# Kernel tuning notes

Measured on AMD Instinct MI355X. Metric: run time of the kernel, lower is better.

## Reference

```python
import jax, jax.numpy as jnp
import numpy as np

N_NODES = 100000
N_EDGES = 1600000
N_GRAPHS = 512
NODE_DIM = 92
EDGE_DIM = 41
H = 64            # hidden_node_dim
NUM_CONV = 3
PRED_H = 128
BN_EPS = 1e-5


def setup_inputs() -> dict:
    key = jax.random.key(0)
    ks = jax.random.split(key, 16)
    inp = {
        "node_feats": jax.random.normal(ks[0], (N_NODES, NODE_DIM), jnp.float32),
        "edge_index": jax.random.randint(ks[1], (2, N_EDGES), 0, N_NODES, jnp.int32),
        "edge_feats": jax.random.normal(ks[2], (N_EDGES, EDGE_DIM), jnp.float32),
        "graph_id": jax.random.randint(ks[3], (N_NODES,), 0, N_GRAPHS, jnp.int32),
        # parameters (scaled like default torch init)
        "emb_W": jax.random.normal(ks[4], (NODE_DIM, H), jnp.float32) / np.sqrt(NODE_DIM),
        "emb_b": jnp.zeros((H,), jnp.float32),
        "conv_W": jax.random.normal(ks[5], (NUM_CONV, 2 * H + EDGE_DIM, 2 * H), jnp.float32) / np.sqrt(2 * H + EDGE_DIM),
        "conv_b": jnp.zeros((NUM_CONV, 2 * H), jnp.float32),
        "bn_gamma": jnp.ones((NUM_CONV, 2 * H), jnp.float32),
        "bn_beta": jnp.zeros((NUM_CONV, 2 * H), jnp.float32),
        "fc_W": jax.random.normal(ks[6], (H, PRED_H), jnp.float32) / np.sqrt(H),
        "fc_b": jnp.zeros((PRED_H,), jnp.float32),
        "out_W": jax.random.normal(ks[7], (PRED_H, 1), jnp.float32) / np.sqrt(PRED_H),
        "out_b": jnp.zeros((1,), jnp.float32),
    }
    return inp


def reference(node_feats, edge_index, edge_feats, graph_id,
              emb_W, emb_b, conv_W, conv_b, bn_gamma, bn_beta,
              fc_W, fc_b, out_W, out_b):
    src = edge_index[0]
    dst = edge_index[1]
    n_nodes = node_feats.shape[0]

    # 1. atom embedding
    h = node_feats @ emb_W + emb_b                         # [N, H]

    # 2. conv layers: gather -> linear -> batchnorm -> gated message -> scatter-add
    for l in range(NUM_CONV):
        z = jnp.concatenate([h[src], h[dst], edge_feats], axis=1)   # [E, 2H+edge_dim]
        z = z @ conv_W[l] + conv_b[l]                                # [E, 2H]
        mean = jnp.mean(z, axis=0)
        var = jnp.var(z, axis=0)                                     # biased, as torch BN training
        z = (z - mean) * jax.lax.rsqrt(var + BN_EPS) * bn_gamma[l] + bn_beta[l]
        msg = jax.nn.sigmoid(z[:, :H]) * jax.nn.softplus(z[:, H:])   # [E, H]
        h = h + jax.ops.segment_sum(msg, src, num_segments=n_nodes)

    # 3. per-crystal mean pooling
    sums = jax.ops.segment_sum(h, graph_id, num_segments=N_GRAPHS)   # [G, H]
    counts = jax.ops.segment_sum(jnp.ones((n_nodes,), h.dtype), graph_id, num_segments=N_GRAPHS)
    pooled = sums / jnp.maximum(counts, 1.0)[:, None]

    # 4. head
    out = jax.nn.softplus(pooled @ fc_W + fc_b)
    return out @ out_W + out_b                                       # [G, 1]
```

## Files before the change

kernel.cpp:

```cpp
#include <hip/hip_runtime.h>
#include <hip/hip_fp16.h>

#define NDIM 92
#define HDIM 64
#define EDIM 41
#define ZC   128
#define CIN  169
#define NB   2048

__global__ __launch_bounds__(256) void k_embed(
    const float* __restrict__ nf, const float* __restrict__ W,
    const float* __restrict__ b, float* __restrict__ h, int N)
{
    __shared__ float Wl[NDIM * HDIM];
    __shared__ float nfl[4][NDIM];
    int t = threadIdx.x;
    for (int i = t; i < NDIM * HDIM; i += 256) Wl[i] = W[i];
    int n0 = blockIdx.x * 4;
    for (int i = t; i < 4 * NDIM; i += 256) {
        int slot = i / NDIM, k = i - slot * NDIM;
        int n = n0 + slot;
        nfl[slot][k] = (n < N) ? nf[n * NDIM + k] : 0.f;
    }
    __syncthreads();
    int j = t & 63, slot = t >> 6;
    int n = n0 + slot;
    if (n >= N) return;
    float acc = b[j];
    #pragma unroll
    for (int k = 0; k < NDIM; k++) acc += nfl[slot][k] * Wl[k * HDIM + j];
    h[n * HDIM + j] = acc;
}

__global__ __launch_bounds__(256) void k_pq(
    const float* __restrict__ h, const float* __restrict__ Wl,
    float* __restrict__ PQ, int N)
{
    __shared__ float Wcat[64 * 256];
    __shared__ float hl[32 * 64];
    int t = threadIdx.x;
    for (int i = t; i < 64 * 256; i += 256) {
        int k = i >> 8, c = i & 255;
        Wcat[i] = (c < 128) ? Wl[k * 128 + c] : Wl[(64 + k) * 128 + (c - 128)];
    }
    int jg = t & 63, w = t >> 6;
    int ntiles = (N + 31) >> 5;
    for (int tile = blockIdx.x; tile < ntiles; tile += gridDim.x) {
        int nbase = tile << 5;
        __syncthreads();
        for (int i = t; i < 32 * 64; i += 256) {
            int nn = nbase + (i >> 6);
            hl[i] = (nn < N) ? h[nn * 64 + (i & 63)] : 0.f;
        }
        __syncthreads();
        float acc[8][4];
        #pragma unroll
        for (int n = 0; n < 8; n++)
            acc[n][0] = acc[n][1] = acc[n][2] = acc[n][3] = 0.f;
        for (int k = 0; k < 64; k++) {
            float4 w4 = *(const float4*)&Wcat[k * 256 + jg * 4];
            #pragma unroll
            for (int n = 0; n < 8; n++) {
                float hv = hl[(w * 8 + n) * 64 + k];
                acc[n][0] += hv * w4.x; acc[n][1] += hv * w4.y;
                acc[n][2] += hv * w4.z; acc[n][3] += hv * w4.w;
            }
        }
        #pragma unroll
        for (int n = 0; n < 8; n++) {
            int nn = nbase + w * 8 + n;
            if (nn < N)
                *(float4*)&PQ[nn * 256 + jg * 4] =
                    make_float4(acc[n][0], acc[n][1], acc[n][2], acc[n][3]);
        }
    }
}

__global__ __launch_bounds__(256) void k_passA(
    const float* __restrict__ PQ, const float* __restrict__ ef,
    const int* __restrict__ src, const int* __restrict__ dst,
    const float* __restrict__ Wl, const float* __restrict__ bias,
    __half* __restrict__ zh, float* __restrict__ partials, int E)
{
    int t = threadIdx.x;
    int lane = t & 63;
    int waveid = __builtin_amdgcn_readfirstlane(t >> 6);
    int pair = waveid >> 1;
    int jcol = ((waveid & 1) << 6) | lane;

    float wreg[EDIM];
    #pragma unroll
    for (int k = 0; k < EDIM; k++) wreg[k] = Wl[(128 + k) * 128 + jcol];
    float bj = bias[jcol];

    float psum = 0.f, psq = 0.f;
    int estep = gridDim.x * 2;
    for (int e = blockIdx.x * 2 + pair; e < E; e += estep) {
        int s = src[e], d = dst[e];
        const float* efe = ef + (size_t)e * EDIM;
        float acc0 = PQ[(size_t)s * 256 + jcol];
        float acc1 = PQ[(size_t)d * 256 + 128 + jcol] + bj;
        #pragma unroll
        for (int k = 0; k < 40; k += 2) {
            acc0 += efe[k]     * wreg[k];
            acc1 += efe[k + 1] * wreg[k + 1];
        }
        acc0 += efe[40] * wreg[40];
        float z = acc0 + acc1;
        zh[(size_t)e * 128 + jcol] = __float2half(z);
        psum += z; psq += z * z;
    }
    __shared__ float red[512];
    red[t] = psum; red[256 + t] = psq;
    __syncthreads();
    if (t < 128) {
        partials[blockIdx.x * 256 + t]       = red[t] + red[t + 128];
        partials[blockIdx.x * 256 + 128 + t] = red[256 + t] + red[256 + t + 128];
    }
}

__global__ __launch_bounds__(256) void k_red1(
    const float* __restrict__ partials, float* __restrict__ p2, int nb)
{
    int t = threadIdx.x, r = blockIdx.x;
    float s = 0.f;
    int b0 = r * 32, b1 = b0 + 32; if (b1 > nb) b1 = nb;
    for (int b = b0; b < b1; b++) s += partials[b * 256 + t];
    p2[r * 256 + t] = s;
}

__global__ __launch_bounds__(256) void k_bnstats(
    const float* __restrict__ p2, const float* __restrict__ gamma,
    const float* __restrict__ beta, float* __restrict__ bnA,
    float* __restrict__ bnC, int R, float invE)
{
    int t = threadIdx.x;
    float s = 0.f;
    for (int r = 0; r < R; r++) s += p2[r * 256 + t];
    __shared__ float red[256];
    red[t] = s;
    __syncthreads();
    if (t < 128) {
        float mean = red[t] * invE;
        float var  = red[128 + t] * invE - mean * mean;
        float a = gamma[t] * rsqrtf(var + 1e-5f);
        bnA[t] = a;
        bnC[t] = beta[t] - mean * a;
    }
}

__global__ __launch_bounds__(256) void k_passB(
    const __half* __restrict__ zh, const int* __restrict__ src,
    const float* __restrict__ bnA, const float* __restrict__ bnC,
    float* __restrict__ h, int E)
{
    int t = threadIdx.x;
    int j = t & 63, slot = t >> 6;
    float a0 = bnA[j],      c0 = bnC[j];
    float a1 = bnA[64 + j], c1 = bnC[64 + j];
    for (int e = blockIdx.x * 4 + slot; e < E; e += gridDim.x * 4) {
        float za = __half2float(zh[e * 128 + j])      * a0 + c0;
        float zb = __half2float(zh[e * 128 + 64 + j]) * a1 + c1;
        float sig = 1.f / (1.f + __expf(-za));
        float sp  = fmaxf(zb, 0.f) + log1pf(__expf(-fabsf(zb)));
        atomicAdd(&h[src[e] * 64 + j], sig * sp);
    }
}

__global__ __launch_bounds__(256) void k_pool(
    const float* __restrict__ h, const int* __restrict__ gid,
    float* __restrict__ pool, float* __restrict__ cnt, int N)
{
    int t = threadIdx.x;
    int j = t & 63, slot = t >> 6;
    int n = blockIdx.x * 4 + slot;
    if (n >= N) return;
    int g = gid[n];
    atomicAdd(&pool[g * 64 + j], h[n * 64 + j]);
    if (j == 0) atomicAdd(&cnt[g], 1.f);
}

__global__ __launch_bounds__(128) void k_head(
    const float* __restrict__ pool, const float* __restrict__ cnt,
    const float* __restrict__ fcW, const float* __restrict__ fcb,
    const float* __restrict__ outW, const float* __restrict__ outb,
    float* __restrict__ out, int G)
{
    int g = blockIdx.x, t = threadIdx.x;
    __shared__ float pl[64];
    if (t < 64) pl[t] = pool[g * 64 + t] / fmaxf(cnt[g], 1.f);
    __syncthreads();
    float acc = fcb[t];
    #pragma unroll
    for (int k = 0; k < 64; k++) acc += pl[k] * fcW[k * 128 + t];
    float sp = fmaxf(acc, 0.f) + log1pf(__expf(-fabsf(acc)));
    float v = sp * outW[t];
    __shared__ float red[128];
    red[t] = v;
    __syncthreads();
    for (int s = 64; s > 0; s >>= 1) {
        if (t < s) red[t] += red[t + s];
        __syncthreads();
    }
    if (t == 0) out[g] = red[0] + outb[0];
}

extern "C" void kernel_launch(void* const* d_in, const int* in_sizes, int n_in,
                              void* d_out, int out_size, void* d_ws, size_t ws_size,
                              hipStream_t stream)
{
    const float* nf    = (const float*)d_in[0];
    const int*   ei    = (const int*)d_in[1];
    const float* ef    = (const float*)d_in[2];
    const int*   gid   = (const int*)d_in[3];
    const float* embW  = (const float*)d_in[4];
    const float* embB  = (const float*)d_in[5];
    const float* convW = (const float*)d_in[6];
    const float* convB = (const float*)d_in[7];
    const float* gam   = (const float*)d_in[8];
    const float* bet   = (const float*)d_in[9];
    const float* fcW   = (const float*)d_in[10];
    const float* fcb   = (const float*)d_in[11];
    const float* outW  = (const float*)d_in[12];
    const float* outb  = (const float*)d_in[13];
    float* out = (float*)d_out;

    int N = in_sizes[0] / NDIM;
    int E = in_sizes[1] / 2;
    int G = out_size;
    const int* src = ei;
    const int* dst = ei + E;

    char* ws = (char*)d_ws;
    size_t off = 0;
    auto alloc = [&](size_t bytes) {
        void* p = ws + off;
        off = (off + bytes + 255) & ~(size_t)255;
        return p;
    };
    float*  h        = (float*)alloc((size_t)N * 64 * 4);
    float*  PQ       = (float*)alloc((size_t)N * 256 * 4);
    __half* zh       = (__half*)alloc((size_t)E * 128 * 2);
    float*  partials = (float*)alloc((size_t)NB * 256 * 4);
    float*  p2       = (float*)alloc((size_t)64 * 256 * 4);
    float*  bnA      = (float*)alloc(128 * 4);
    float*  bnC      = (float*)alloc(128 * 4);
    float*  pool     = (float*)alloc((size_t)G * 65 * 4);
    float*  cnt      = pool + (size_t)G * 64;

    k_embed<<<(N + 3) / 4, 256, 0, stream>>>(nf, embW, embB, h, N);

    for (int l = 0; l < 3; l++) {
        const float* Wl = convW + (size_t)l * CIN * ZC;
        k_pq<<<1024, 256, 0, stream>>>(h, Wl, PQ, N);
        k_passA<<<NB, 256, 0, stream>>>(PQ, ef, src, dst, Wl, convB + l * ZC,
                                        zh, partials, E);
        k_red1<<<64, 256, 0, stream>>>(partials, p2, NB);
        k_bnstats<<<1, 256, 0, stream>>>(p2, gam + l * ZC, bet + l * ZC,
                                         bnA, bnC, 64, 1.f / (float)E);
        k_passB<<<4096, 256, 0, stream>>>(zh, src, bnA, bnC, h, E);
    }

    hipMemsetAsync(pool, 0, (size_t)G * 65 * 4, stream);
    k_pool<<<(N + 3) / 4, 256, 0, stream>>>(h, gid, pool, cnt, N);
    k_head<<<G, 128, 0, stream>>>(pool, cnt, fcW, fcb, outW, outb, out, G);
}
```

Measured before the change: 4.321 ms.

## Compute edge-feature projection in passA with bf16 MFMA tiles

```diff
diff --git a/kernel.cpp b/kernel.cpp
--- a/kernel.cpp
+++ b/kernel.cpp
@@ -7,6 +7,15 @@
 #define ZC   128
 #define CIN  169
 #define NB   2048
+
+typedef __attribute__((ext_vector_type(8))) short short8;
+typedef __attribute__((ext_vector_type(4))) float f32x4;
+
+static __device__ inline unsigned short f2bf(float x) {
+    unsigned u = __float_as_uint(x);
+    unsigned r = (u + 0x7FFF + ((u >> 16) & 1)) >> 16;
+    return (unsigned short)r;
+}
 
 __global__ __launch_bounds__(256) void k_embed(
     const float* __restrict__ nf, const float* __restrict__ W,
@@ -76,41 +85,105 @@
     }
 }
 
+__global__ __launch_bounds__(64) void k_wswz(
+    const float* __restrict__ Wl, unsigned short* __restrict__ Wsw)
+{
+    int b = blockIdx.x;
+    int ks = b >> 3, nt = b & 7;
+    int lane = threadIdx.x;
+    #pragma unroll
+    for (int i = 0; i < 8; i++) {
+        int k = ks * 32 + ((lane >> 4) * 8) + i;
+        int n = nt * 16 + (lane & 15);
+        float v = (k < EDIM) ? Wl[(128 + k) * 128 + n] : 0.f;
+        Wsw[((size_t)(ks * 8 + nt) * 64 + lane) * 8 + i] = f2bf(v);
+    }
+}
+
 __global__ __launch_bounds__(256) void k_passA(
     const float* __restrict__ PQ, const float* __restrict__ ef,
     const int* __restrict__ src, const int* __restrict__ dst,
-    const float* __restrict__ Wl, const float* __restrict__ bias,
+    const unsigned short* __restrict__ Wsw, const float* __restrict__ bias,
     __half* __restrict__ zh, float* __restrict__ partials, int E)
 {
+    __shared__ unsigned short efl[64 * 72];
+    __shared__ __half Rl[64 * 128];
+    __shared__ float red[512];
+
     int t = threadIdx.x;
     int lane = t & 63;
-    int waveid = __builtin_amdgcn_readfirstlane(t >> 6);
-    int pair = waveid >> 1;
-    int jcol = ((waveid & 1) << 6) | lane;
-
-    float wreg[EDIM];
+    int w = t >> 6;
+    int jcol = t & 127;
+    int slot = t >> 7;
+
+    short8 bfr[2][8];
     #pragma unroll
-    for (int k = 0; k < EDIM; k++) wreg[k] = Wl[(128 + k) * 128 + jcol];
+    for (int ks = 0; ks < 2; ks++)
+        #pragma unroll
+        for (int nt = 0; nt < 8; nt++)
+            bfr[ks][nt] = *(const short8*)(Wsw + ((size_t)(ks * 8 + nt) * 64 + lane) * 8);
+
     float bj = bias[jcol];
-
     float psum = 0.f, psq = 0.f;
-    int estep = gridDim.x * 2;
-    for (int e = blockIdx.x * 2 + pair; e < E; e += estep) {
-        int s = src[e], d = dst[e];
-        const float* efe = ef + (size_t)e * EDIM;
-        float acc0 = PQ[(size_t)s * 256 + jcol];
-        float acc1 = PQ[(size_t)d * 256 + 128 + jcol] + bj;
-        #pragma unroll
-        for (int k = 0; k < 40; k += 2) {
-            acc0 += efe[k]     * wreg[k];
-            acc1 += efe[k + 1] * wreg[k + 1];
-        }
-        acc0 += efe[40] * wreg[40];
-        float z = acc0 + acc1;
-        zh[(size_t)e * 128 + jcol] = __float2half(z);
-        psum += z; psq += z * z;
-    }
-    __shared__ float red[512];
+
+    int arow = (w * 16 + (lane & 15));
+    int aq   = (lane >> 4) * 8;
+    int crow = w * 16 + (lane >> 4) * 4;
+    int ccol = lane & 15;
+
+    int ntiles = (E + 63) >> 6;
+    for (int tile = blockIdx.x; tile < ntiles; tile += gridDim.x) {
+        int e0 = tile << 6;
+        __syncthreads();
+        #pragma unroll
+        for (int s = 0; s < 8; s++) {
+            int idx = s * 256 + t;
+            int row = idx >> 5, q = idx & 31;
+            int e = e0 + row;
+            int k0 = q * 2;
+            unsigned pack = 0;
+            if (e < E) {
+                float v0 = (k0 < EDIM) ? ef[(size_t)e * EDIM + k0] : 0.f;
+                float v1 = (k0 + 1 < EDIM) ? ef[(size_t)e * EDIM + k0 + 1] : 0.f;
+                pack = (unsigned)f2bf(v0) | ((unsigned)f2bf(v1) << 16);
+            }
+            ((unsigned*)efl)[row * 36 + q] = pack;
+        }
+        __syncthreads();
+        {
+            short8 a0 = *(const short8*)(efl + arow * 72 + aq);
+            short8 a1 = *(const short8*)(efl + arow * 72 + 32 + aq);
+            f32x4 acc[8];
+            #pragma unroll
+            for (int nt = 0; nt < 8; nt++) {
+                acc[nt] = (f32x4){0.f, 0.f, 0.f, 0.f};
+                acc[nt] = __builtin_amdgcn_mfma_f32_16x16x32_bf16(a0, bfr[0][nt], acc[nt], 0, 0, 0);
+                acc[nt] = __builtin_amdgcn_mfma_f32_16x16x32_bf16(a1, bfr[1][nt], acc[nt], 0, 0, 0);
+            }
+            #pragma unroll
+            for (int nt = 0; nt < 8; nt++)
+                #pragma unroll
+                for (int r = 0; r < 4; r++)
+                    Rl[(crow + r) * 128 + nt * 16 + ccol] = __float2half(acc[nt][r]);
+        }
+        __syncthreads();
+        #pragma unroll
+        for (int i2 = 0; i2 < 64; i2 += 8) {
+            #pragma unroll
+            for (int u = 0; u < 4; u++) {
+                int el = i2 + u * 2 + slot;
+                int e = e0 + el;
+                if (e < E) {
+                    int s = src[e], d = dst[e];
+                    float z = __half2float(Rl[el * 128 + jcol])
+                            + PQ[(size_t)s * 256 + jcol]
+                            + PQ[(size_t)d * 256 + 128 + jcol] + bj;
+                    zh[(size_t)e * 128 + jcol] = __float2half(z);
+                    psum += z; psq += z * z;
+                }
+            }
+        }
+    }
     red[t] = psum; red[256 + t] = psq;
     __syncthreads();
     if (t < 128) {
@@ -159,11 +232,11 @@
     float a0 = bnA[j],      c0 = bnC[j];
     float a1 = bnA[64 + j], c1 = bnC[64 + j];
     for (int e = blockIdx.x * 4 + slot; e < E; e += gridDim.x * 4) {
-        float za = __half2float(zh[e * 128 + j])      * a0 + c0;
-        float zb = __half2float(zh[e * 128 + 64 + j]) * a1 + c1;
+        float za = __half2float(zh[(size_t)e * 128 + j])      * a0 + c0;
+        float zb = __half2float(zh[(size_t)e * 128 + 64 + j]) * a1 + c1;
         float sig = 1.f / (1.f + __expf(-za));
         float sp  = fmaxf(zb, 0.f) + log1pf(__expf(-fabsf(zb)));
-        atomicAdd(&h[src[e] * 64 + j], sig * sp);
+        atomicAdd(&h[(size_t)src[e] * 64 + j], sig * sp);
     }
 }
 
@@ -245,6 +318,7 @@
     float*  p2       = (float*)alloc((size_t)64 * 256 * 4);
     float*  bnA      = (float*)alloc(128 * 4);
     float*  bnC      = (float*)alloc(128 * 4);
+    unsigned short* Wsw = (unsigned short*)alloc(16384);
     float*  pool     = (float*)alloc((size_t)G * 65 * 4);
     float*  cnt      = pool + (size_t)G * 64;
 
@@ -253,7 +327,8 @@
     for (int l = 0; l < 3; l++) {
         const float* Wl = convW + (size_t)l * CIN * ZC;
         k_pq<<<1024, 256, 0, stream>>>(h, Wl, PQ, N);
-        k_passA<<<NB, 256, 0, stream>>>(PQ, ef, src, dst, Wl, convB + l * ZC,
+        k_wswz<<<16, 64, 0, stream>>>(Wl, Wsw);
+        k_passA<<<NB, 256, 0, stream>>>(PQ, ef, src, dst, Wsw, convB + l * ZC,
                                         zh, partials, E);
         k_red1<<<64, 256, 0, stream>>>(partials, p2, NB);
         k_bnstats<<<1, 256, 0, stream>>>(p2, gam + l * ZC, bet + l * ZC,
```

After: 5.596 ms. 1.3x slower.
